# Optimization experiments

Hardware: AMD Instinct MI355X
Metric: run time of the kernel (lower is better)

## Reference

```python
import jax, jax.numpy as jnp
import numpy as np

B, TD, ND, FD, H = 16384, 256, 256, 512, 8
HID = [512, 256]


def _ln(x, g, b, eps=1e-5):
    m = jnp.mean(x, -1, keepdims=True)
    v = jnp.mean((x - m) ** 2, -1, keepdims=True)
    return (x - m) * jax.lax.rsqrt(v + eps) * g + b


def _mha1(q_in, k_in, v_in, wq, bq, wk, bk, wv, bv, wo, bo):
    # MultiheadAttention with seq_len=1 on both sides; eval mode (dropout off).
    Bq, E = q_in.shape
    dh = E // H
    q = (q_in @ wq.T + bq).reshape(Bq, H, dh)
    k = (k_in @ wk.T + bk).reshape(Bq, H, dh)
    scores = jnp.sum(q * k, -1) / np.sqrt(dh)          # [B, H]
    w = jax.nn.softmax(scores[..., None], axis=-1)      # [B, H, 1] -> exactly 1 (single key)
    attn = jnp.mean(w, axis=1)[:, None, :]              # averaged over heads -> [B, 1, 1]
    v = v_in @ wv.T + bv                                # attn weight == 1, so attn_out == v
    out = v @ wo.T + bo
    return out, attn


def setup_inputs():
    key = jax.random.key(0)
    ks = iter(jax.random.split(key, 40))
    def p(*shape):
        return jax.random.normal(next(ks), shape, dtype=jnp.float32) * 0.02
    inp = {
        'text_emb': jax.random.normal(next(ks), (B, TD), dtype=jnp.float32),
        'num_emb': jax.random.normal(next(ks), (B, ND), dtype=jnp.float32),
        'tp_w': p(FD, TD), 'tp_b': p(FD),
        'np_w': p(FD, ND), 'np_b': p(FD),
        'a1_wq': p(FD, FD), 'a1_wk': p(FD, FD), 'a1_wv': p(FD, FD),
        'a1_bq': p(FD), 'a1_bk': p(FD), 'a1_bv': p(FD),
        'a1_wo': p(FD, FD), 'a1_bo': p(FD),
        'a2_wq': p(FD, FD), 'a2_wk': p(FD, FD), 'a2_wv': p(FD, FD),
        'a2_bq': p(FD), 'a2_bk': p(FD), 'a2_bv': p(FD),
        'a2_wo': p(FD, FD), 'a2_bo': p(FD),
        'n1_g': jnp.ones((FD,), jnp.float32), 'n1_b': jnp.zeros((FD,), jnp.float32),
        'n2_g': jnp.ones((FD,), jnp.float32), 'n2_b': jnp.zeros((FD,), jnp.float32),
        'g_w': p(FD, 2 * FD), 'g_b': p(FD),
        'm1_w': p(HID[0], 2 * FD), 'm1_b': p(HID[0]),
        'ln1_g': jnp.ones((HID[0],), jnp.float32), 'ln1_b': jnp.zeros((HID[0],), jnp.float32),
        'm2_w': p(HID[1], HID[0]), 'm2_b': p(HID[1]),
        'ln2_g': jnp.ones((HID[1],), jnp.float32), 'ln2_b': jnp.zeros((HID[1],), jnp.float32),
    }
    return inp


def reference(text_emb, num_emb, tp_w, tp_b, np_w, np_b,
              a1_wq, a1_wk, a1_wv, a1_bq, a1_bk, a1_bv, a1_wo, a1_bo,
              a2_wq, a2_wk, a2_wv, a2_bq, a2_bk, a2_bv, a2_wo, a2_bo,
              n1_g, n1_b, n2_g, n2_b, g_w, g_b,
              m1_w, m1_b, ln1_g, ln1_b, m2_w, m2_b, ln2_g, ln2_b):
    t = text_emb @ tp_w.T + tp_b                        # [B, FD]
    n = num_emb @ np_w.T + np_b                         # [B, FD]
    n2t, attn_n2t = _mha1(n, t, t, a1_wq, a1_bq, a1_wk, a1_bk, a1_wv, a1_bv, a1_wo, a1_bo)
    n2t = _ln(n + n2t, n1_g, n1_b)
    t2n, attn_t2n = _mha1(t, n, n, a2_wq, a2_bq, a2_wk, a2_bk, a2_wv, a2_bv, a2_wo, a2_bo)
    t2n = _ln(t + t2n, n2_g, n2_b)
    comb = jnp.concatenate([n2t, t2n], axis=-1)         # [B, 2*FD]
    gate = jax.nn.sigmoid(comb @ g_w.T + g_b)           # [B, FD]
    h = jax.nn.gelu(_ln(comb @ m1_w.T + m1_b, ln1_g, ln1_b), approximate=False)
    fused = jax.nn.gelu(_ln(h @ m2_w.T + m2_b, ln2_g, ln2_b), approximate=False)
    return fused, gate, attn_n2t, attn_t2n
```

## Files before the change

### kernel.cpp

```cpp
#include <hip/hip_runtime.h>
#include <math.h>

typedef unsigned short u16;
typedef __bf16 bf16x8 __attribute__((ext_vector_type(8)));
typedef float f32x4 __attribute__((ext_vector_type(4)));
typedef short s16x8 __attribute__((ext_vector_type(8)));
typedef short s16x4 __attribute__((ext_vector_type(4)));

__device__ __forceinline__ float b2f(u16 u) {
    union { unsigned i; float f; } c; c.i = ((unsigned)u) << 16; return c.f;
}
__device__ __forceinline__ u16 f2b(float f) {
    union { float f; unsigned i; } c; c.f = f;
    return (u16)((c.i + 0x7fffu + ((c.i >> 16) & 1u)) >> 16);
}
__device__ __forceinline__ float gelu_f(float v) {
    return 0.5f * v * (1.0f + erff(v * 0.70710678118654752f));
}
__device__ __forceinline__ void async_cp16(const u16* g, u16* l) {
    __builtin_amdgcn_global_load_lds((const __attribute__((address_space(1))) void*)g,
                                     (__attribute__((address_space(3))) void*)l, 16, 0, 0);
}

template<int SUBN>
__global__ __launch_bounds__(256, 2)
void gemm_bt(const u16* __restrict__ A0, const u16* __restrict__ A1,
             const u16* __restrict__ W0, const u16* __restrict__ W1,
             const float* __restrict__ B0, const float* __restrict__ B1,
             const float* __restrict__ LG0, const float* __restrict__ LB0,
             const float* __restrict__ LG1, const float* __restrict__ LB1,
             void* __restrict__ O0v, void* __restrict__ O1v,
             int lda, int K, int halfBlocks, int ldo0, int ldo1,
             int mode0, int mode1)
{
    constexpr int NCOL = 256 * SUBN;
    constexpr int EPIW = NCOL + 8;
    constexpr int STAGE = (64 + NCOL) * 64;
    constexpr int EPIS = 64 * EPIW;
    __shared__ u16 sm[STAGE > EPIS ? STAGE : EPIS];
    u16* sA = sm;
    u16* sW = sm + 64 * 64;

    const int bx = blockIdx.x, by = blockIdx.y;
    const int half = (bx >= halfBlocks) ? 1 : 0;
    const int bxl = bx - half * halfBlocks;
    const u16* A = (half ? A1 : A0) + (size_t)by * 64 * lda;
    const u16* W = (half ? W1 : W0) + (size_t)bxl * NCOL * K;
    const float* bias = half ? B1 : B0;
    const float* lng = half ? LG1 : LG0;
    const float* lnb = half ? LB1 : LB0;
    void* outv = half ? O1v : O0v;
    const int ldo = half ? ldo1 : ldo0;
    const int mode = half ? mode1 : mode0;

    const int tid = threadIdx.x;
    const int lane = tid & 63;
    const int wave = tid >> 6;
    const int fc = lane & 15;
    const int quad = lane >> 4;

    int par[2], pac[2];
#pragma unroll
    for (int c = 0; c < 2; ++c) {
        const int p = tid + 256 * c;
        par[c] = p >> 3;
        pac[c] = ((p & 7) - (par[c] & 7)) & 7;
    }
    constexpr int WCH = 8 * SUBN;
    int pwr[WCH], pwc[WCH];
#pragma unroll
    for (int c = 0; c < WCH; ++c) {
        const int p = tid + 256 * c;
        pwr[c] = p >> 3;
        pwc[c] = ((p & 7) - (pwr[c] & 7)) & 7;
    }

    f32x4 acc[4][4 * SUBN];
#pragma unroll
    for (int i = 0; i < 4; ++i)
#pragma unroll
        for (int j = 0; j < 4 * SUBN; ++j)
            acc[i][j] = f32x4{0.f, 0.f, 0.f, 0.f};

    for (int k0 = 0; k0 < K; k0 += 64) {
#pragma unroll
        for (int c = 0; c < 2; ++c)
            async_cp16(A + (size_t)par[c] * lda + k0 + pac[c] * 8, &sA[(tid + 256 * c) * 8]);
#pragma unroll
        for (int c = 0; c < WCH; ++c)
            async_cp16(W + (size_t)pwr[c] * K + k0 + pwc[c] * 8, &sW[(tid + 256 * c) * 8]);
        __syncthreads();

#pragma unroll
        for (int kk = 0; kk < 2; ++kk) {
            bf16x8 af[4];
#pragma unroll
            for (int i = 0; i < 4; ++i) {
                const int ar = i * 16 + fc;
                const int slot = ar * 8 + ((kk * 4 + quad + (ar & 7)) & 7);
                af[i] = *(const bf16x8*)&sA[slot * 8];
            }
#pragma unroll
            for (int sub = 0; sub < SUBN; ++sub) {
                bf16x8 wf[4];
#pragma unroll
                for (int j = 0; j < 4; ++j) {
                    const int wr = wave * 64 * SUBN + sub * 64 + j * 16 + fc;
                    const int slot = wr * 8 + ((kk * 4 + quad + (wr & 7)) & 7);
                    wf[j] = *(const bf16x8*)&sW[slot * 8];
                }
#pragma unroll
                for (int i = 0; i < 4; ++i)
#pragma unroll
                    for (int j = 0; j < 4; ++j)
                        acc[i][sub * 4 + j] =
                            __builtin_amdgcn_mfma_f32_16x16x32_bf16(af[i], wf[j], acc[i][sub * 4 + j], 0, 0, 0);
            }
        }
        __syncthreads();
    }

    const int colb = bxl * NCOL;

    if (mode <= 1) {
#pragma unroll
        for (int sub = 0; sub < SUBN; ++sub)
#pragma unroll
        for (int j = 0; j < 4; ++j) {
            const int colh = colb + wave * 64 * SUBN + sub * 64 + j * 16 + fc;
            const float bv = bias[colh];
#pragma unroll
            for (int i = 0; i < 4; ++i)
#pragma unroll
            for (int r = 0; r < 4; ++r) {
                const int row = by * 64 + i * 16 + quad * 4 + r;
                const float v = acc[i][sub * 4 + j][r] + bv;
                if (mode == 1)
                    ((float*)outv)[(size_t)row * ldo + colh] = 1.0f / (1.0f + expf(-v));
                else
                    ((u16*)outv)[(size_t)row * ldo + colh] = f2b(v);
            }
        }
    } else {
        float bb[SUBN * 4];
#pragma unroll
        for (int sub = 0; sub < SUBN; ++sub)
#pragma unroll
        for (int j = 0; j < 4; ++j)
            bb[sub * 4 + j] = bias[colb + wave * 64 * SUBN + sub * 64 + j * 16 + fc];
#pragma unroll
        for (int sub = 0; sub < SUBN; ++sub)
#pragma unroll
        for (int j = 0; j < 4; ++j) {
            const int col = wave * 64 * SUBN + sub * 64 + j * 16 + fc;
#pragma unroll
            for (int i = 0; i < 4; ++i)
#pragma unroll
            for (int r = 0; r < 4; ++r)
                sm[(i * 16 + quad * 4 + r) * EPIW + col] =
                    f2b(acc[i][sub * 4 + j][r] + bb[sub * 4 + j]);
        }
        __syncthreads();

        constexpr int CE = NCOL / 64;
        constexpr float INV = 1.0f / (float)NCOL;
        float gv[CE], bvv[CE];
#pragma unroll
        for (int e = 0; e < CE; ++e) {
            gv[e] = lng[lane * CE + e];
            bvv[e] = lnb[lane * CE + e];
        }
        for (int rr = 0; rr < 16; ++rr) {
            const int rl = wave * 16 + rr;
            const int grow = by * 64 + rl;
            float x[CE], s = 0.f, ss = 0.f;
            if constexpr (CE == 8) {
                s16x8 xv = *(const s16x8*)&sm[rl * EPIW + lane * 8];
#pragma unroll
                for (int e = 0; e < 8; ++e) { x[e] = b2f((u16)xv[e]); s += x[e]; ss += x[e] * x[e]; }
            } else {
                s16x4 xv = *(const s16x4*)&sm[rl * EPIW + lane * 4];
#pragma unroll
                for (int e = 0; e < 4; ++e) { x[e] = b2f((u16)xv[e]); s += x[e]; ss += x[e] * x[e]; }
            }
#pragma unroll
            for (int m = 32; m >= 1; m >>= 1) { s += __shfl_xor(s, m, 64); ss += __shfl_xor(ss, m, 64); }
            const float mean = s * INV;
            const float var = ss * INV - mean * mean;
            const float rs = rsqrtf(var + 1e-5f);
            float y[CE];
#pragma unroll
            for (int e = 0; e < CE; ++e) {
                y[e] = (x[e] - mean) * rs * gv[e] + bvv[e];
                if (mode >= 3) y[e] = gelu_f(y[e]);
            }
            if (mode == 4) {
                float* o = (float*)outv;
#pragma unroll
                for (int e = 0; e < CE; ++e)
                    o[(size_t)grow * ldo + colb + lane * CE + e] = y[e];
                if (lane == 0) {
                    o[(size_t)16384 * 768 + grow] = 1.0f;
                    o[(size_t)16384 * 769 + grow] = 1.0f;
                }
            } else {
                u16* o = (u16*)outv;
                if constexpr (CE == 8) {
                    s16x8 ov;
#pragma unroll
                    for (int e = 0; e < 8; ++e) ov[e] = (short)f2b(y[e]);
                    *(s16x8*)&o[(size_t)grow * ldo + colb + lane * 8] = ov;
                } else {
                    s16x4 ov;
#pragma unroll
                    for (int e = 0; e < 4; ++e) ov[e] = (short)f2b(y[e]);
                    *(s16x4*)&o[(size_t)grow * ldo + colb + lane * 4] = ov;
                }
            }
        }
    }
}


__device__ __forceinline__ void cvt_quads(const float* __restrict__ src,
                                          u16* __restrict__ dst, int bi, int tid)
{
#pragma unroll
    for (int c = 0; c < 2; ++c) {
        const int q = bi * 512 + tid + 256 * c;
        f32x4 v = *(const f32x4*)(src + (size_t)q * 4);
        s16x4 o;
        o[0] = (short)f2b(v[0]); o[1] = (short)f2b(v[1]);
        o[2] = (short)f2b(v[2]); o[3] = (short)f2b(v[3]);
        *(s16x4*)(dst + (size_t)q * 4) = o;
    }
}

__device__ void transpose_cvt64(const float* __restrict__ src, int C,
                                u16* __restrict__ dst, int R,
                                int tr, int tc, int tid, float* sm)
{
    const int lr = tid >> 4, lc4 = (tid & 15) * 4;
#pragma unroll
    for (int m = 0; m < 4; ++m) {
        const int i = lr + m * 16;
        f32x4 v = *(const f32x4*)&src[(size_t)(tr + i) * C + tc + lc4];
#pragma unroll
        for (int mm = 0; mm < 4; ++mm) sm[i * 65 + lc4 + mm] = v[mm];
    }
    __syncthreads();
#pragma unroll
    for (int m = 0; m < 4; ++m) {
        const int j = lr + m * 16;
        s16x4 o;
#pragma unroll
        for (int mm = 0; mm < 4; ++mm)
            o[mm] = (short)f2b(sm[(size_t)(lc4 + mm) * 65 + j]);
        *(s16x4*)&dst[(size_t)(tc + j) * R + tr + lc4] = o;
    }
}

__device__ void matvec_rows(const float* __restrict__ M, const float* __restrict__ v,
                            const float* __restrict__ add1, const float* __restrict__ add2,
                            float* __restrict__ out, int r0, int tid, float* sm)
{
    for (int i = tid; i < 512; i += 256) sm[i] = v[i];
    __syncthreads();
    const int row = r0 + (tid & 63), q = tid >> 6;
    float s = 0.f;
    for (int k = q * 128; k < q * 128 + 128; k += 4) {
        f32x4 m = *(const f32x4*)&M[(size_t)row * 512 + k];
        s += m[0] * sm[k] + m[1] * sm[k + 1] + m[2] * sm[k + 2] + m[3] * sm[k + 3];
    }
    sm[512 + tid] = s;
    __syncthreads();
    if (tid < 64)
        out[r0 + tid] = sm[512 + tid] + sm[512 + tid + 64] + sm[512 + tid + 128] +
                        sm[512 + tid + 192] + add1[r0 + tid] + add2[r0 + tid];
}

__global__ __launch_bounds__(256)
void prep_cvt(const float* __restrict__ text, const float* __restrict__ num,
              const float* __restrict__ tp_w, const float* __restrict__ np_w,
              const float* __restrict__ g_w, const float* __restrict__ m1_w,
              const float* __restrict__ m2_w,
              const float* __restrict__ a1_wv, const float* __restrict__ a2_wv,
              const float* __restrict__ a1_wo, const float* __restrict__ a2_wo,
              const float* __restrict__ a1_bv, const float* __restrict__ a1_bo,
              const float* __restrict__ a2_bv, const float* __restrict__ a2_bo,
              const float* __restrict__ tp_b, const float* __restrict__ np_b,
              u16* __restrict__ EMBc, u16* __restrict__ Wbig,
              u16* __restrict__ g_bf, u16* __restrict__ m1_bf, u16* __restrict__ m2_bf,
              u16* __restrict__ a1_wvT, u16* __restrict__ a2_wvT,
              u16* __restrict__ tp_wT, u16* __restrict__ np_wT,
              u16* __restrict__ a1_wo_bf, u16* __restrict__ a2_wo_bf,
              float* __restrict__ w1, float* __restrict__ w2,
              float* __restrict__ zb)
{
    __shared__ float smem[64 * 65];
    const int b = blockIdx.x, tid = threadIdx.x;
    if (b < 4096) {
#pragma unroll
        for (int c = 0; c < 2; ++c) {
            const int q = b * 512 + tid + 256 * c;
            const int e = q * 4, row = e >> 9, col = e & 511;
            const float* src = (col < 256) ? text + (size_t)row * 256 + col
                                           : num + (size_t)row * 256 + (col - 256);
            f32x4 v = *(const f32x4*)src;
            s16x4 o;
            o[0] = (short)f2b(v[0]); o[1] = (short)f2b(v[1]);
            o[2] = (short)f2b(v[2]); o[3] = (short)f2b(v[3]);
            *(s16x4*)(EMBc + e) = o;
        }
    } else if (b < 4352) { cvt_quads(g_w, g_bf, b - 4096, tid); }
    else if (b < 4608) { cvt_quads(m1_w, m1_bf, b - 4352, tid); }
    else if (b < 4672) { cvt_quads(m2_w, m2_bf, b - 4608, tid); }
    else if (b < 4736) {
#pragma unroll
        for (int c = 0; c < 2; ++c) {
            const int q = (b - 4672) * 512 + tid + 256 * c;
            const int e = q * 4, row = e >> 8, col = e & 255;
            f32x4 v = *(const f32x4*)(np_w + e);
            s16x4 o;
            o[0] = (short)f2b(v[0]); o[1] = (short)f2b(v[1]);
            o[2] = (short)f2b(v[2]); o[3] = (short)f2b(v[3]);
            *(s16x4*)(Wbig + (size_t)row * 512 + 256 + col) = o;
        }
    } else if (b < 4800) {
#pragma unroll
        for (int c = 0; c < 2; ++c) {
            const int q = (b - 4736) * 512 + tid + 256 * c;
            const int e = q * 4, row = e >> 8, col = e & 255;
            f32x4 v = *(const f32x4*)(tp_w + e);
            s16x4 o;
            o[0] = (short)f2b(v[0]); o[1] = (short)f2b(v[1]);
            o[2] = (short)f2b(v[2]); o[3] = (short)f2b(v[3]);
            *(s16x4*)(Wbig + (size_t)(512 + row) * 512 + col) = o;
        }
    } else if (b < 4864) {
        const int t = b - 4800;
        transpose_cvt64(a1_wv, 512, a1_wvT, 512, (t >> 3) * 64, (t & 7) * 64, tid, smem);
    } else if (b < 4928) {
        const int t = b - 4864;
        transpose_cvt64(a2_wv, 512, a2_wvT, 512, (t >> 3) * 64, (t & 7) * 64, tid, smem);
    } else if (b < 4960) {
        const int t = b - 4928;
        transpose_cvt64(tp_w, 256, tp_wT, 512, (t >> 2) * 64, (t & 3) * 64, tid, smem);
    } else if (b < 4992) {
        const int t = b - 4960;
        transpose_cvt64(np_w, 256, np_wT, 512, (t >> 2) * 64, (t & 3) * 64, tid, smem);
    } else if (b < 5120) { cvt_quads(a1_wo, a1_wo_bf, b - 4992, tid); }
    else if (b < 5248) { cvt_quads(a2_wo, a2_wo_bf, b - 5120, tid); }
    else if (b < 5256) {
        matvec_rows(a1_wo, a1_bv, a1_bo, np_b, w1, (b - 5248) * 64, tid, smem);
    } else if (b < 5264) {
        matvec_rows(a2_wo, a2_bv, a2_bo, tp_b, w2, (b - 5256) * 64, tid, smem);
    } else {
        *(f32x4*)&zb[tid * 4] = f32x4{0.f, 0.f, 0.f, 0.f};
    }
}

__global__ __launch_bounds__(256)
void prep_bias(const u16* __restrict__ M1, const u16* __restrict__ M2,
               const float* __restrict__ tp_b, const float* __restrict__ np_b,
               const float* __restrict__ w1, const float* __restrict__ w2,
               float* __restrict__ bbig)
{
    __shared__ float sm[768];
    const int b = blockIdx.x, tid = threadIdx.x;
    const int side = b >> 3, r0 = (b & 7) * 64;
    const u16* M = side ? M2 : M1;
    const float* v = side ? np_b : tp_b;
    const float* w = side ? w2 : w1;
    float* out = bbig + side * 512;
    for (int i = tid; i < 512; i += 256) sm[i] = v[i];
    __syncthreads();
    const int row = r0 + (tid & 63), q = tid >> 6;
    float s = 0.f;
    for (int k = q * 128; k < q * 128 + 128; k += 8) {
        s16x8 m = *(const s16x8*)&M[(size_t)row * 512 + k];
#pragma unroll
        for (int j = 0; j < 8; ++j) s += b2f((u16)m[j]) * sm[k + j];
    }
    sm[512 + tid] = s;
    __syncthreads();
    if (tid < 64)
        out[r0 + tid] = sm[512 + tid] + sm[512 + tid + 64] + sm[512 + tid + 128] +
                        sm[512 + tid + 192] + w[r0 + tid];
}

extern "C" void kernel_launch(void* const* d_in, const int* in_sizes, int n_in,
                              void* d_out, int out_size, void* d_ws, size_t ws_size,
                              hipStream_t stream)
{
    const float* text  = (const float*)d_in[0];
    const float* num   = (const float*)d_in[1];
    const float* tp_w  = (const float*)d_in[2];
    const float* tp_b  = (const float*)d_in[3];
    const float* np_w  = (const float*)d_in[4];
    const float* np_b  = (const float*)d_in[5];
    const float* a1_wv = (const float*)d_in[8];
    const float* a1_bv = (const float*)d_in[11];
    const float* a1_wo = (const float*)d_in[12];
    const float* a1_bo = (const float*)d_in[13];
    const float* a2_wv = (const float*)d_in[16];
    const float* a2_bv = (const float*)d_in[19];
    const float* a2_wo = (const float*)d_in[20];
    const float* a2_bo = (const float*)d_in[21];
    const float* n1_g  = (const float*)d_in[22];
    const float* n1_b  = (const float*)d_in[23];
    const float* n2_g  = (const float*)d_in[24];
    const float* n2_b  = (const float*)d_in[25];
    const float* g_w   = (const float*)d_in[26];
    const float* g_b   = (const float*)d_in[27];
    const float* m1_w  = (const float*)d_in[28];
    const float* m1_b  = (const float*)d_in[29];
    const float* ln1_g = (const float*)d_in[30];
    const float* ln1_b = (const float*)d_in[31];
    const float* m2_w  = (const float*)d_in[32];
    const float* m2_b  = (const float*)d_in[33];
    const float* ln2_g = (const float*)d_in[34];
    const float* ln2_b = (const float*)d_in[35];

    float* outp = (float*)d_out;
    char* ob = (char*)d_out;
    char* ws = (char*)d_ws;
    const size_t KB = 1024, MB = 1048576;

    u16* Wbig    = (u16*)(ob);
    u16* g_bf    = (u16*)(ob + 1 * MB);
    u16* m1_bf   = (u16*)(ob + 2 * MB);
    u16* a1_wvT  = (u16*)(ob + 3 * MB + 256 * KB);
    u16* a2_wvT  = (u16*)(ob + 3 * MB + 768 * KB);
    u16* tp_wT   = (u16*)(ob + 4 * MB + 256 * KB);
    u16* np_wT   = (u16*)(ob + 4 * MB + 512 * KB);
    u16* a1_wo_bf= (u16*)(ob + 4 * MB + 768 * KB);
    u16* a2_wo_bf= (u16*)(ob + 5 * MB + 256 * KB);
    u16* M1      = (u16*)(ob + 5 * MB + 768 * KB);
    u16* M2      = (u16*)(ob + 6 * MB + 256 * KB);
    float* w1    = (float*)(ob + 6 * MB + 768 * KB);
    float* w2    = w1 + 512;
    float* bbig  = w1 + 1024;
    float* zb    = w1 + 2048;
    u16* EMBc    = (u16*)(ob + 16 * MB);
    u16* X     = (u16*)ws;
    u16* m2_bf = (u16*)(ws + 32 * MB);
    u16* h     = (u16*)(ws + 48 * MB);

    dim3 blk(256);

    prep_cvt<<<5265, blk, 0, stream>>>(text, num, tp_w, np_w, g_w, m1_w, m2_w,
        a1_wv, a2_wv, a1_wo, a2_wo, a1_bv, a1_bo, a2_bv, a2_bo, tp_b, np_b,
        EMBc, Wbig, g_bf, m1_bf, m2_bf, a1_wvT, a2_wvT, tp_wT, np_wT,
        a1_wo_bf, a2_wo_bf, w1, w2, zb);
    gemm_bt<2><<<dim3(2, 8), blk, 0, stream>>>(a1_wo_bf, a2_wo_bf, a1_wvT, a2_wvT,
        zb, zb, nullptr, nullptr, nullptr, nullptr,
        M1, M2, 512, 512, 1, 512, 512, 0, 0);
    prep_bias<<<16, blk, 0, stream>>>(M1, M2, tp_b, np_b, w1, w2, bbig);
    gemm_bt<1><<<dim3(2, 8), blk, 0, stream>>>(M1, M2, tp_wT, np_wT,
        zb, zb, nullptr, nullptr, nullptr, nullptr,
        Wbig, Wbig + (size_t)512 * 512 + 256, 512, 512, 1, 512, 512, 0, 0);
    gemm_bt<2><<<dim3(2, 256), blk, 0, stream>>>(EMBc, EMBc,
        Wbig, Wbig + (size_t)512 * 512, bbig, bbig + 512,
        n1_g, n1_b, n2_g, n2_b,
        X, X + 512, 512, 512, 1, 1024, 1024, 2, 2);
    gemm_bt<2><<<dim3(2, 256), blk, 0, stream>>>(X, X, g_bf, m1_bf, g_b, m1_b,
        nullptr, nullptr, ln1_g, ln1_b,
        outp + (size_t)16384 * 256, h, 1024, 1024, 1, 512, 512, 1, 3);
    gemm_bt<1><<<dim3(1, 256), blk, 0, stream>>>(h, h, m2_bf, m2_bf, m2_b, m2_b,
        ln2_g, ln2_b, ln2_g, ln2_b,
        outp, outp, 512, 512, 1, 256, 256, 4, 4);
}
```

Before: 319.6 us.

## Double-buffer GEMM LDS staging with 32-wide K tiles and async prefetch

The GEMM main loop now uses two LDS buffers with K-tiles of 32 instead of one buffer with K-tiles of 64. The next tile is prefetched through global_load_lds while the current tile's MFMAs run, which removes one of the two barriers per iteration and overlaps load latency with compute. Swizzled LDS offsets are precomputed once into registers. The trade-offs are twice as many loop iterations, each with less work per barrier, more registers for the offsets, and an extra barrier before the epilogue reuses shared memory. Total LDS size stays about the same.

```diff
diff --git a/kernel.cpp b/kernel.cpp
--- a/kernel.cpp
+++ b/kernel.cpp
@@ -34,12 +34,11 @@
              int mode0, int mode1)
 {
     constexpr int NCOL = 256 * SUBN;
+    constexpr int WCH  = NCOL / 64;
+    constexpr int BUFE = (64 + NCOL) * 32;
     constexpr int EPIW = NCOL + 8;
-    constexpr int STAGE = (64 + NCOL) * 64;
     constexpr int EPIS = 64 * EPIW;
-    __shared__ u16 sm[STAGE > EPIS ? STAGE : EPIS];
-    u16* sA = sm;
-    u16* sW = sm + 64 * 64;
+    __shared__ u16 sm[(2 * BUFE > EPIS) ? 2 * BUFE : EPIS];
 
     const int bx = blockIdx.x, by = blockIdx.y;
     const int half = (bx >= halfBlocks) ? 1 : 0;
@@ -59,20 +58,31 @@
     const int fc = lane & 15;
     const int quad = lane >> 4;
 
-    int par[2], pac[2];
-#pragma unroll
-    for (int c = 0; c < 2; ++c) {
-        const int p = tid + 256 * c;
-        par[c] = p >> 3;
-        pac[c] = ((p & 7) - (par[c] & 7)) & 7;
-    }
-    constexpr int WCH = 8 * SUBN;
-    int pwr[WCH], pwc[WCH];
+    int arw, ac8;
+    { const int hi = tid >> 3, t7 = ((tid & 7) - hi) & 7; arw = (hi << 1) + (t7 >> 2); ac8 = t7 & 3; }
+    int wrw[WCH], wc8[WCH];
 #pragma unroll
     for (int c = 0; c < WCH; ++c) {
         const int p = tid + 256 * c;
-        pwr[c] = p >> 3;
-        pwc[c] = ((p & 7) - (pwr[c] & 7)) & 7;
+        const int hi = p >> 3, t7 = ((p & 7) - hi) & 7;
+        wrw[c] = (hi << 1) + (t7 >> 2); wc8[c] = t7 & 3;
+    }
+
+    int aoff[4];
+#pragma unroll
+    for (int i = 0; i < 4; ++i) {
+        const int ar = i * 16 + fc;
+        const int s = ((ar >> 1) << 3) + ((((ar & 1) << 2) + quad + (ar >> 1)) & 7);
+        aoff[i] = s * 8;
+    }
+    int woff[4 * SUBN];
+#pragma unroll
+    for (int sub = 0; sub < SUBN; ++sub)
+#pragma unroll
+    for (int j = 0; j < 4; ++j) {
+        const int wr = wave * (64 * SUBN) + sub * 64 + j * 16 + fc;
+        const int s = ((wr >> 1) << 3) + ((((wr & 1) << 2) + quad + (wr >> 1)) & 7);
+        woff[sub * 4 + j] = s * 8;
     }
 
     f32x4 acc[4][4 * SUBN];
@@ -82,43 +92,45 @@
         for (int j = 0; j < 4 * SUBN; ++j)
             acc[i][j] = f32x4{0.f, 0.f, 0.f, 0.f};
 
-    for (int k0 = 0; k0 < K; k0 += 64) {
-#pragma unroll
-        for (int c = 0; c < 2; ++c)
-            async_cp16(A + (size_t)par[c] * lda + k0 + pac[c] * 8, &sA[(tid + 256 * c) * 8]);
+    auto STAGE = [&](int b, int k0) {
+        u16* base = sm + b * BUFE;
+        async_cp16(A + (size_t)arw * lda + k0 + ac8 * 8, base + tid * 8);
 #pragma unroll
         for (int c = 0; c < WCH; ++c)
-            async_cp16(W + (size_t)pwr[c] * K + k0 + pwc[c] * 8, &sW[(tid + 256 * c) * 8]);
+            async_cp16(W + (size_t)wrw[c] * K + k0 + wc8[c] * 8,
+                       base + 64 * 32 + (tid + 256 * c) * 8);
+    };
+    auto COMPUTE = [&](int b) {
+        const u16* bA = sm + b * BUFE;
+        const u16* bW = bA + 64 * 32;
+        bf16x8 af[4];
+#pragma unroll
+        for (int i = 0; i < 4; ++i) af[i] = *(const bf16x8*)&bA[aoff[i]];
+#pragma unroll
+        for (int sub = 0; sub < SUBN; ++sub) {
+            bf16x8 wf[4];
+#pragma unroll
+            for (int j = 0; j < 4; ++j) wf[j] = *(const bf16x8*)&bW[woff[sub * 4 + j]];
+#pragma unroll
+            for (int i = 0; i < 4; ++i)
+#pragma unroll
+            for (int j = 0; j < 4; ++j)
+                acc[i][sub * 4 + j] =
+                    __builtin_amdgcn_mfma_f32_16x16x32_bf16(af[i], wf[j], acc[i][sub * 4 + j], 0, 0, 0);
+        }
+    };
+
+    const int NT = K >> 5;
+    STAGE(0, 0);
+    __syncthreads();
+    int cur = 0;
+    for (int t = 0; t < NT - 1; ++t) {
+        STAGE(cur ^ 1, (t + 1) << 5);
+        COMPUTE(cur);
         __syncthreads();
-
-#pragma unroll
-        for (int kk = 0; kk < 2; ++kk) {
-            bf16x8 af[4];
-#pragma unroll
-            for (int i = 0; i < 4; ++i) {
-                const int ar = i * 16 + fc;
-                const int slot = ar * 8 + ((kk * 4 + quad + (ar & 7)) & 7);
-                af[i] = *(const bf16x8*)&sA[slot * 8];
-            }
-#pragma unroll
-            for (int sub = 0; sub < SUBN; ++sub) {
-                bf16x8 wf[4];
-#pragma unroll
-                for (int j = 0; j < 4; ++j) {
-                    const int wr = wave * 64 * SUBN + sub * 64 + j * 16 + fc;
-                    const int slot = wr * 8 + ((kk * 4 + quad + (wr & 7)) & 7);
-                    wf[j] = *(const bf16x8*)&sW[slot * 8];
-                }
-#pragma unroll
-                for (int i = 0; i < 4; ++i)
-#pragma unroll
-                    for (int j = 0; j < 4; ++j)
-                        acc[i][sub * 4 + j] =
-                            __builtin_amdgcn_mfma_f32_16x16x32_bf16(af[i], wf[j], acc[i][sub * 4 + j], 0, 0, 0);
-            }
-        }
-        __syncthreads();
-    }
+        cur ^= 1;
+    }
+    COMPUTE(cur);
 
     const int colb = bxl * NCOL;
 
@@ -142,6 +154,7 @@
             }
         }
     } else {
+        __syncthreads();
         float bb[SUBN * 4];
 #pragma unroll
         for (int sub = 0; sub < SUBN; ++sub)
```

Measured after the change: 337.4 us. +5.6%, slower.
